# Performance work log

Hardware: AMD Instinct MI355X
Metric: run time of the kernel (lower is better)

The kernel has to match this reference:

```python
import jax, jax.numpy as jnp
import numpy as np

N = 50000        # nodes
E = 500000       # undirected edges (stored once)
D = 64           # n_in_features
DOUT = 64        # n_out_features
HLF = 2          # hl_factor
NCONV = 3        # n_conv_its
H = D * HLF      # hidden width of conv MLPs


def setup_inputs() -> dict:
    key = jax.random.key(0)
    ks = jax.random.split(key, 8)
    s = 0.05
    edge_features = jax.random.normal(ks[0], (E, D), jnp.float32)
    edge_index = jax.random.randint(ks[1], (2, E), 0, N, dtype=jnp.int64)
    node_w1 = jax.random.normal(ks[2], (NCONV, 2 * D, H), jnp.float32) * s
    node_b1 = jnp.zeros((NCONV, H), jnp.float32)
    node_w2 = jax.random.normal(ks[3], (NCONV, H, D), jnp.float32) * s
    node_b2 = jnp.zeros((NCONV, D), jnp.float32)
    edge_w1 = jax.random.normal(ks[4], (2 * D, H), jnp.float32) * s
    edge_b1 = jnp.zeros((H,), jnp.float32)
    edge_w2 = jax.random.normal(ks[5], (H, DOUT), jnp.float32) * s
    edge_b2 = jnp.zeros((DOUT,), jnp.float32)
    return dict(edge_features=edge_features, edge_index=edge_index,
                node_w1=node_w1, node_b1=node_b1, node_w2=node_w2, node_b2=node_b2,
                edge_w1=edge_w1, edge_b1=edge_b1, edge_w2=edge_w2, edge_b2=edge_b2)


def _seg_mean(x, idx, n):
    s = jax.ops.segment_sum(x, idx, num_segments=n)
    c = jax.ops.segment_sum(jnp.ones((idx.shape[0], 1), x.dtype), idx, num_segments=n)
    return s / jnp.maximum(c, 1.0)


def reference(edge_features, edge_index, node_w1, node_b1, node_w2, node_b2,
              edge_w1, edge_b1, edge_w2, edge_b2):
    src, dst = edge_index[0], edge_index[1]
    # bidirectional (symmetrized) edges for message passing
    bi_src = jnp.concatenate([src, dst])
    bi_dst = jnp.concatenate([dst, src])

    # EdgeConvNoNodes: node feature = mean of incident edge features
    x = _seg_mean(jnp.concatenate([edge_features, edge_features], axis=0), bi_dst, N)  # [N, D]

    # NodeConv layers with residual: message = MLP(cat[x_i, x_j]), mean-aggregated
    for i in range(NCONV):
        m = jnp.concatenate([x[bi_dst], x[bi_src]], axis=-1)        # [2E, 2D]
        m = jax.nn.relu(m @ node_w1[i] + node_b1[i])                # [2E, H]
        m = jax.nn.relu(m @ node_w2[i] + node_b2[i])                # [2E, D]
        x = x + _seg_mean(m, bi_dst, N)

    # EdgeConv: symmetric edge MLP over node endpoint pairs + symmetry side loss
    def emlp(a, b):
        h = jax.nn.relu(jnp.concatenate([a, b], axis=-1) @ edge_w1 + edge_b1)
        return h @ edge_w2 + edge_b2

    e1 = emlp(x[src], x[dst])   # [E, DOUT]
    e2 = emlp(x[dst], x[src])   # [E, DOUT]
    edge_out = 0.5 * (e1 + e2)
    side_loss = jnp.mean((e1 - e2) ** 2)
    return edge_out, side_loss
```

## Files before the change

kernel.cpp:

```cpp
#include <hip/hip_runtime.h>


#define NN 50000
#define NE 500000
#define DE 1000000
#define NEB 7813

typedef __attribute__((ext_vector_type(8))) __bf16 bfrag;
typedef __attribute__((ext_vector_type(8))) short  svec8;
typedef __attribute__((ext_vector_type(4))) float  f32x4;

__device__ __forceinline__ unsigned short f2bf(float f){
  unsigned u = __builtin_bit_cast(unsigned, f);
  u += 0x7fffu + ((u >> 16) & 1u);
  return (unsigned short)(u >> 16);
}
__device__ __forceinline__ float bf2f(unsigned short s){
  return __builtin_bit_cast(float, ((unsigned)s) << 16);
}
#define MFMA __builtin_amdgcn_mfma_f32_16x16x32_bf16

__device__ __forceinline__ bfrag hbuild(const unsigned short* __restrict__ p,
                                        const unsigned short* __restrict__ q){
  svec8 pv = *(const svec8*)p;
  svec8 qv = *(const svec8*)q;
  bfrag r;
  #pragma unroll
  for (int i = 0; i < 8; i++){
    float f = bf2f((unsigned short)pv[i]) + bf2f((unsigned short)qv[i]);
    f = f > 0.f ? f : 0.f;
    r[i] = (__bf16)f;
  }
  return r;
}

__global__ void k_hist(const int* __restrict__ ei, int* __restrict__ cnt){
  int e = blockIdx.x*256 + threadIdx.x;
  if (e >= DE) return;
  int dst = (e < NE) ? ei[NE + e] : ei[e - NE];
  atomicAdd(&cnt[dst], 1);
}

__global__ void k_scan(const int* __restrict__ cnt, int* __restrict__ off,
                       int* __restrict__ cur, float* __restrict__ dinv){
  __shared__ int wsum[16];
  __shared__ int carry_s;
  int tid = threadIdx.x;
  int lane = tid & 63, w = tid >> 6;
  int carry = 0;
  for (int base = 0; base < NN; base += 1024){
    int idx = base + tid;
    int v = (idx < NN) ? cnt[idx] : 0;
    int inc = v;
    for (int o2 = 1; o2 < 64; o2 <<= 1){
      int t = __shfl_up(inc, o2);
      if (lane >= o2) inc += t;
    }
    if (lane == 63) wsum[w] = inc;
    __syncthreads();
    if (tid < 16){
      int vv = wsum[tid], p = vv;
      for (int o2 = 1; o2 < 16; o2 <<= 1){
        int t = __shfl_up(p, o2, 16);
        if (tid >= o2) p += t;
      }
      wsum[tid] = p - vv;
    }
    __syncthreads();
    int ex = carry + wsum[w] + inc - v;
    if (idx < NN){
      off[idx] = ex; cur[idx] = ex;
      dinv[idx] = 1.0f / (float)(v > 1 ? v : 1);
    }
    if (tid == 1023) carry_s = carry + wsum[15] + inc;
    __syncthreads();
    carry = carry_s;
  }
  if (tid == 0) off[NN] = DE;
}

__global__ void k_fill(const int* __restrict__ ei, int* __restrict__ cur,
                       int* __restrict__ nbr, int* __restrict__ dstA, int* __restrict__ eid){
  int e = blockIdx.x*256 + threadIdx.x;
  if (e >= DE) return;
  int s, d, id;
  if (e < NE){ s = ei[e];  d = ei[NE + e]; id = e;      }
  else       { s = ei[e];  d = ei[e - NE]; id = e - NE; }
  int pos = atomicAdd(&cur[d], 1);
  nbr[pos] = s; dstA[pos] = d; eid[pos] = id;
}

__global__ void k_pack(const float* __restrict__ nw1, const float* __restrict__ nw2,
                       const float* __restrict__ ew1, const float* __restrict__ ew2,
                       unsigned short* __restrict__ wp){
  int t = blockIdx.x*256 + threadIdx.x;
  if (t >= 98304) return;
  const float* src; int NO, p, base;
  if (t < 49152)      { int l = t/16384;            src = nw1 + l*16384; NO=128; p = t - l*16384;      base = t - p; }
  else if (t < 73728) { int q = t-49152; int l=q/8192; src = nw2 + l*8192; NO=64; p = q - l*8192;      base = t - p; }
  else if (t < 90112) {                              src = ew1;           NO=128; p = t - 73728;       base = 73728; }
  else                {                              src = ew2;           NO=64;  p = t - 90112;       base = 90112; }
  int f = p >> 9, r = p & 511, lane = r >> 3, i = r & 7;
  int NB = NO >> 4, kb = f / NB, nb = f - kb*NB;
  int k = kb*32 + ((lane >> 4) << 3) + i;
  int c = nb*16 + (lane & 15);
  wp[base + p] = f2bf(src[k*NO + c]);
}

__global__ __launch_bounds__(256,4) void k_init(
    const float* __restrict__ ef, const int* __restrict__ dstA,
    const int* __restrict__ eid, float* __restrict__ xsum)
{
  int lane = threadIdx.x & 63, wid = threadIdx.x >> 6;
  int tile = (blockIdx.x*4 + wid) * 32;
  if (tile >= DE) return;
  int q = lane >> 4, c4 = lane & 15;
  int dr = dstA[tile + (lane & 31)];
  int er = eid[tile + (lane & 31)];
  f32x4 v[8];
  #pragma unroll
  for (int it = 0; it < 8; it++){
    int row = q + it*4;
    int e = __shfl(er, row);
    v[it] = *(const f32x4*)(ef + (size_t)e*64 + c4*4);
  }
  int prev = __shfl_up(dr, 1);
  bool flag = (lane < 32) && (lane == 0 || dr != prev);
  unsigned long long mask = __ballot(flag);
  while (mask){
    int s = (int)__builtin_ctzll(mask);
    mask &= mask - 1;
    int e = mask ? (int)__builtin_ctzll(mask) : 32;
    int dseg = __shfl(dr, s);
    f32x4 p = {0,0,0,0};
    #pragma unroll
    for (int it = 0; it < 8; it++){
      int row = q + it*4;
      if ((unsigned)(row - s) < (unsigned)(e - s)) p += v[it];
    }
    #pragma unroll
    for (int k = 0; k < 4; k++){
      p[k] += __shfl_xor(p[k], 16);
      p[k] += __shfl_xor(p[k], 32);
    }
    if (q == 0){
      atomicAdd(&xsum[dseg*64 + c4*4 + 0], p[0]);
      atomicAdd(&xsum[dseg*64 + c4*4 + 1], p[1]);
      atomicAdd(&xsum[dseg*64 + c4*4 + 2], p[2]);
      atomicAdd(&xsum[dseg*64 + c4*4 + 3], p[3]);
    }
  }
}

__global__ void k_div(const float* __restrict__ xsum, const float* __restrict__ dinv,
                      float* __restrict__ x, unsigned short* __restrict__ xbf){
  int n = blockIdx.x*4 + (threadIdx.x >> 6);
  int lane = threadIdx.x & 63;
  if (n >= NN) return;
  float v = xsum[n*64 + lane] * dinv[n];
  x[n*64 + lane] = v;
  xbf[n*64 + lane] = f2bf(v);
}

__global__ __launch_bounds__(256,2) void k_pq(
    const unsigned short* __restrict__ xbf,
    const unsigned short* __restrict__ wp, int w1off,
    const float* __restrict__ bias,
    unsigned short* __restrict__ pb, unsigned short* __restrict__ qb)
{
  int lane = threadIdx.x & 63, wid = threadIdx.x >> 6;
  int tile = (blockIdx.x*4 + wid) * 32;
  if (tile >= NN) return;
  int r16 = lane & 15, g = lane >> 4;
  const svec8* w1g = (const svec8*)(wp + w1off);
  bfrag a[2][2];
  #pragma unroll
  for (int rb = 0; rb < 2; rb++){
    int n = tile + rb*16 + r16; if (n >= NN) n = NN-1;
    #pragma unroll
    for (int kb = 0; kb < 2; kb++)
      a[rb][kb] = __builtin_bit_cast(bfrag, *(const svec8*)(xbf + n*64 + kb*32 + g*8));
  }
  for (int ph = 0; ph < 2; ph++){
    f32x4 acc[8][2];
    #pragma unroll
    for (int nb = 0; nb < 8; nb++){ acc[nb][0] = (f32x4){0,0,0,0}; acc[nb][1] = (f32x4){0,0,0,0}; }
    #pragma unroll
    for (int kb = 0; kb < 2; kb++){
      #pragma unroll
      for (int nb = 0; nb < 8; nb++){
        bfrag b = __builtin_bit_cast(bfrag, w1g[((ph*2+kb)*8+nb)*64 + lane]);
        acc[nb][0] = MFMA(a[0][kb], b, acc[nb][0], 0, 0, 0);
        acc[nb][1] = MFMA(a[1][kb], b, acc[nb][1], 0, 0, 0);
      }
    }
    unsigned short* ob = ph ? qb : pb;
    #pragma unroll
    for (int nb = 0; nb < 8; nb++){
      float bv = (ph == 0) ? bias[nb*16 + r16] : 0.f;
      #pragma unroll
      for (int rb = 0; rb < 2; rb++){
        #pragma unroll
        for (int j = 0; j < 4; j++){
          int n = tile + rb*16 + g*4 + j;
          if (n < NN) ob[n*128 + nb*16 + r16] = f2bf(acc[nb][rb][j] + bv);
        }
      }
    }
  }
}

__global__ __launch_bounds__(256,4) void k_conv(
    const unsigned short* __restrict__ pb, const unsigned short* __restrict__ qb,
    const int* __restrict__ cdst, const int* __restrict__ cnbr,
    const unsigned short* __restrict__ wp, int w2off,
    const float* __restrict__ b2, float* __restrict__ xsum)
{
  int lane = threadIdx.x & 63, wid = threadIdx.x >> 6;
  int tile = (blockIdx.x*4 + wid) * 32;
  if (tile >= DE) return;
  int r16 = lane & 15, g = lane >> 4;
  int dr = cdst[tile + (lane & 31)];
  int d0 = cdst[tile + r16],      d1 = cdst[tile + 16 + r16];
  int s0 = cnbr[tile + r16],      s1 = cnbr[tile + 16 + r16];
  const svec8* w2g = (const svec8*)(wp + w2off);

  f32x4 acc[4][2];
  #pragma unroll
  for (int nb = 0; nb < 4; nb++){ acc[nb][0] = (f32x4){0,0,0,0}; acc[nb][1] = (f32x4){0,0,0,0}; }

  #pragma unroll
  for (int kb = 0; kb < 4; kb++){
    int off = kb*32 + g*8;
    bfrag h0 = hbuild(pb + d0*128 + off, qb + s0*128 + off);
    bfrag h1 = hbuild(pb + d1*128 + off, qb + s1*128 + off);
    #pragma unroll
    for (int nb = 0; nb < 4; nb++){
      bfrag b = __builtin_bit_cast(bfrag, w2g[(kb*4+nb)*64 + lane]);
      acc[nb][0] = MFMA(h0, b, acc[nb][0], 0, 0, 0);
      acc[nb][1] = MFMA(h1, b, acc[nb][1], 0, 0, 0);
    }
  }
  float m[4][2][4];
  #pragma unroll
  for (int nb = 0; nb < 4; nb++){
    float bv = b2[nb*16 + r16];
    #pragma unroll
    for (int rb = 0; rb < 2; rb++){
      #pragma unroll
      for (int j = 0; j < 4; j++){
        float v = acc[nb][rb][j] + bv;
        m[nb][rb][j] = v > 0.f ? v : 0.f;
      }
    }
  }
  int prev = __shfl_up(dr, 1);
  bool flag = (lane < 32) && (lane == 0 || dr != prev);
  unsigned long long mask = __ballot(flag);
  while (mask){
    int s = (int)__builtin_ctzll(mask);
    mask &= mask - 1;
    int e = mask ? (int)__builtin_ctzll(mask) : 32;
    int dseg = __shfl(dr, s);
    float p0 = 0.f, p1 = 0.f, p2 = 0.f, p3 = 0.f;
    #pragma unroll
    for (int rb = 0; rb < 2; rb++){
      #pragma unroll
      for (int j = 0; j < 4; j++){
        int row = rb*16 + g*4 + j;
        if ((unsigned)(row - s) < (unsigned)(e - s)){
          p0 += m[0][rb][j]; p1 += m[1][rb][j]; p2 += m[2][rb][j]; p3 += m[3][rb][j];
        }
      }
    }
    p0 += __shfl_xor(p0, 16); p0 += __shfl_xor(p0, 32);
    p1 += __shfl_xor(p1, 16); p1 += __shfl_xor(p1, 32);
    p2 += __shfl_xor(p2, 16); p2 += __shfl_xor(p2, 32);
    p3 += __shfl_xor(p3, 16); p3 += __shfl_xor(p3, 32);
    if (g == 0){
      atomicAdd(&xsum[dseg*64 +      r16], p0);
      atomicAdd(&xsum[dseg*64 + 16 + r16], p1);
      atomicAdd(&xsum[dseg*64 + 32 + r16], p2);
      atomicAdd(&xsum[dseg*64 + 48 + r16], p3);
    }
  }
}

__global__ void k_finish(const float* __restrict__ xsum, const float* __restrict__ dinv,
                         float* __restrict__ x, unsigned short* __restrict__ xbf){
  int n = blockIdx.x*4 + (threadIdx.x >> 6);
  int lane = threadIdx.x & 63;
  if (n >= NN) return;
  float v = x[n*64 + lane] + xsum[n*64 + lane] * dinv[n];
  x[n*64 + lane] = v;
  xbf[n*64 + lane] = f2bf(v);
}

__global__ __launch_bounds__(256,4) void k_edge(
    const unsigned short* __restrict__ pe, const unsigned short* __restrict__ qe,
    const int* __restrict__ ei,
    const unsigned short* __restrict__ wp,
    const float* __restrict__ b2,
    float* __restrict__ outp, float* __restrict__ part)
{
  __shared__ float wred[4];
  int lane = threadIdx.x & 63, wid = threadIdx.x >> 6;
  int tile = (blockIdx.x*4 + wid) * 16;
  bool valid = tile < NE;
  int tl = valid ? tile : 0;
  int r16 = lane & 15, g = lane >> 4;
  const svec8* w2g = (const svec8*)(wp + 90112);
  int el = tl + r16;
  int sn = ei[el], dn = ei[NE + el];

  f32x4 acc[4][2];
  #pragma unroll
  for (int nb = 0; nb < 4; nb++){ acc[nb][0] = (f32x4){0,0,0,0}; acc[nb][1] = (f32x4){0,0,0,0}; }

  #pragma unroll
  for (int kb = 0; kb < 4; kb++){
    int off = kb*32 + g*8;
    bfrag h0 = hbuild(pe + sn*128 + off, qe + dn*128 + off);
    bfrag h1 = hbuild(pe + dn*128 + off, qe + sn*128 + off);
    #pragma unroll
    for (int nb = 0; nb < 4; nb++){
      bfrag b = __builtin_bit_cast(bfrag, w2g[(kb*4+nb)*64 + lane]);
      acc[nb][0] = MFMA(h0, b, acc[nb][0], 0, 0, 0);
      acc[nb][1] = MFMA(h1, b, acc[nb][1], 0, 0, 0);
    }
  }
  float lsum = 0.f;
  #pragma unroll
  for (int nb = 0; nb < 4; nb++){
    float bv = b2[nb*16 + r16];
    #pragma unroll
    for (int j = 0; j < 4; j++){
      float v1 = acc[nb][0][j] + bv;
      float v2 = acc[nb][1][j] + bv;
      int e = tile + g*4 + j;
      if (valid) outp[e*64 + nb*16 + r16] = 0.5f*(v1 + v2);
      float d = v1 - v2; lsum += d*d;
    }
  }
  if (!valid) lsum = 0.f;
  for (int o2 = 32; o2 > 0; o2 >>= 1) lsum += __shfl_down(lsum, o2);
  if (lane == 0) wred[wid] = lsum;
  __syncthreads();
  if (threadIdx.x == 0) part[blockIdx.x] = wred[0] + wred[1] + wred[2] + wred[3];
}

__global__ void k_final(const float* __restrict__ part, float* __restrict__ outp){
  __shared__ float wred[16];
  int tid = threadIdx.x;
  float s = 0.f;
  for (int i = tid; i < NEB; i += 1024) s += part[i];
  for (int o2 = 32; o2 > 0; o2 >>= 1) s += __shfl_down(s, o2);
  int lane = tid & 63, w = tid >> 6;
  if (lane == 0) wred[w] = s;
  __syncthreads();
  if (tid == 0){
    float t = 0.f;
    #pragma unroll
    for (int i = 0; i < 16; i++) t += wred[i];
    outp[32000000] = t * (1.0f / 32000000.0f);
  }
}

extern "C" void kernel_launch(void* const* d_in, const int* in_sizes, int n_in,
                              void* d_out, int out_size, void* d_ws, size_t ws_size,
                              hipStream_t stream)
{
  const float* ef  = (const float*)d_in[0];
  const int*   ei  = (const int*)  d_in[1];
  const float* nw1 = (const float*)d_in[2];
  const float* nb1 = (const float*)d_in[3];
  const float* nw2 = (const float*)d_in[4];
  const float* nb2 = (const float*)d_in[5];
  const float* ew1 = (const float*)d_in[6];
  const float* eb1 = (const float*)d_in[7];
  const float* ew2 = (const float*)d_in[8];
  const float* eb2 = (const float*)d_in[9];
  float* outp = (float*)d_out;

  char* ws = (char*)d_ws;
  size_t o = 0;
  auto alloc = [&](size_t b)->char*{ char* p = ws + o; o += (b + 255) & ~(size_t)255; return p; };
  int*   cnt  = (int*)  alloc((size_t)NN*4);
  int*   off  = (int*)  alloc((size_t)(NN+1)*4);
  int*   cur  = (int*)  alloc((size_t)NN*4);
  float* dinv = (float*)alloc((size_t)NN*4);
  int*   nbr  = (int*)  alloc((size_t)DE*4);
  int*   dstA = (int*)  alloc((size_t)DE*4);
  int*   eid  = (int*)  alloc((size_t)DE*4);
  float* x    = (float*)alloc((size_t)NN*64*4);
  unsigned short* xbf = (unsigned short*)alloc((size_t)NN*64*2);
  unsigned short* wp  = (unsigned short*)alloc((size_t)98304*2);
  float* part = (float*)alloc((size_t)NEB*4);
  unsigned short* pbuf = (unsigned short*)alloc((size_t)NN*128*2);
  unsigned short* qbuf = (unsigned short*)alloc((size_t)NN*128*2);
  float* xsI  = (float*)alloc((size_t)NN*64*4);
  float* xs0  = (float*)alloc((size_t)NN*64*4);
  float* xs1  = (float*)alloc((size_t)NN*64*4);
  float* xs2  = (float*)alloc((size_t)NN*64*4);
  float* xsum[3] = {xs0, xs1, xs2};

  hipMemsetAsync(cnt, 0, (size_t)NN*4, stream);
  hipMemsetAsync(xsI, 0, (size_t)NN*64*4, stream);
  hipMemsetAsync(xs0, 0, (size_t)NN*64*4, stream);
  hipMemsetAsync(xs1, 0, (size_t)NN*64*4, stream);
  hipMemsetAsync(xs2, 0, (size_t)NN*64*4, stream);
  k_hist<<<(DE+255)/256, 256, 0, stream>>>(ei, cnt);
  k_scan<<<1, 1024, 0, stream>>>(cnt, off, cur, dinv);
  k_fill<<<(DE+255)/256, 256, 0, stream>>>(ei, cur, nbr, dstA, eid);
  k_pack<<<384, 256, 0, stream>>>(nw1, nw2, ew1, ew2, wp);
  k_init<<<NEB, 256, 0, stream>>>(ef, dstA, eid, xsI);
  k_div<<<NN/4 + 1, 256, 0, stream>>>(xsI, dinv, x, xbf);
  for (int l = 0; l < 3; l++){
    k_pq<<<391, 256, 0, stream>>>(xbf, wp, l*16384, nb1 + l*128, pbuf, qbuf);
    k_conv<<<DE/128 + 1, 256, 0, stream>>>(pbuf, qbuf, dstA, nbr, wp,
                                           49152 + l*8192, nb2 + l*64, xsum[l]);
    k_finish<<<NN/4 + 1, 256, 0, stream>>>(xsum[l], dinv, x, xbf);
  }
  k_pq<<<391, 256, 0, stream>>>(xbf, wp, 73728, eb1, pbuf, qbuf);
  k_edge<<<NEB, 256, 0, stream>>>(pbuf, qbuf, ei, wp, eb2, outp, part);
  k_final<<<1, 1024, 0, stream>>>(part, outp);
}
```

Baseline: 700.1 us.

## Interleave P/Q node buffers, sort final edges by source, batch gathers before MFMA

Merges the separate P and Q node projection buffers into one interleaved [N,256] array so each node's P and Q halves sit on adjacent cache lines. Adds a second CSR-style sort of the original edges by source node so the final edge kernel gathers with more locality, then scatters outputs back through a permutation. Hoists all gathers in k_conv and k_edge ahead of the MFMA loop to expose memory-level parallelism, lowering the occupancy hint from 4 to 3 to make room for the extra registers. This adds a histogram, scan and fill pass plus extra index arrays, and the output writes in k_edge become scattered.

Result: slower. 723.4 us (+3.3%).

```diff
diff --git a/kernel.cpp b/kernel.cpp
--- a/kernel.cpp
+++ b/kernel.cpp
@@ -20,10 +20,7 @@
 }
 #define MFMA __builtin_amdgcn_mfma_f32_16x16x32_bf16
 
-__device__ __forceinline__ bfrag hbuild(const unsigned short* __restrict__ p,
-                                        const unsigned short* __restrict__ q){
-  svec8 pv = *(const svec8*)p;
-  svec8 qv = *(const svec8*)q;
+__device__ __forceinline__ bfrag hbuild2(svec8 pv, svec8 qv){
   bfrag r;
   #pragma unroll
   for (int i = 0; i < 8; i++){
@@ -34,15 +31,18 @@
   return r;
 }
 
-__global__ void k_hist(const int* __restrict__ ei, int* __restrict__ cnt){
+__global__ void k_hist(const int* __restrict__ ei, int* __restrict__ cnt,
+                       int* __restrict__ cnt2){
   int e = blockIdx.x*256 + threadIdx.x;
   if (e >= DE) return;
   int dst = (e < NE) ? ei[NE + e] : ei[e - NE];
   atomicAdd(&cnt[dst], 1);
-}
-
-__global__ void k_scan(const int* __restrict__ cnt, int* __restrict__ off,
-                       int* __restrict__ cur, float* __restrict__ dinv){
+  if (e < NE) atomicAdd(&cnt2[ei[e]], 1);
+}
+
+__device__ __forceinline__ void scan_impl(const int* __restrict__ cnt,
+                                          int* __restrict__ off, int* __restrict__ cur,
+                                          float* __restrict__ dinv, int total){
   __shared__ int wsum[16];
   __shared__ int carry_s;
   int tid = threadIdx.x;
@@ -76,11 +76,21 @@
     __syncthreads();
     carry = carry_s;
   }
-  if (tid == 0) off[NN] = DE;
+  if (tid == 0) off[NN] = total;
+}
+
+__global__ void k_scan2(const int* __restrict__ cntA, int* __restrict__ offA,
+                        int* __restrict__ curA, float* __restrict__ dinvA,
+                        const int* __restrict__ cntB, int* __restrict__ offB,
+                        int* __restrict__ curB, float* __restrict__ dinvB){
+  if (blockIdx.x == 0) scan_impl(cntA, offA, curA, dinvA, DE);
+  else                 scan_impl(cntB, offB, curB, dinvB, NE);
 }
 
 __global__ void k_fill(const int* __restrict__ ei, int* __restrict__ cur,
-                       int* __restrict__ nbr, int* __restrict__ dstA, int* __restrict__ eid){
+                       int* __restrict__ nbr, int* __restrict__ dstA, int* __restrict__ eid,
+                       int* __restrict__ cur2, int* __restrict__ eord,
+                       int* __restrict__ es, int* __restrict__ ed){
   int e = blockIdx.x*256 + threadIdx.x;
   if (e >= DE) return;
   int s, d, id;
@@ -88,6 +98,10 @@
   else       { s = ei[e];  d = ei[e - NE]; id = e - NE; }
   int pos = atomicAdd(&cur[d], 1);
   nbr[pos] = s; dstA[pos] = d; eid[pos] = id;
+  if (e < NE){
+    int p2 = atomicAdd(&cur2[s], 1);
+    eord[p2] = e; es[p2] = s; ed[p2] = d;
+  }
 }
 
 __global__ void k_pack(const float* __restrict__ nw1, const float* __restrict__ nw2,
@@ -166,7 +180,7 @@
     const unsigned short* __restrict__ xbf,
     const unsigned short* __restrict__ wp, int w1off,
     const float* __restrict__ bias,
-    unsigned short* __restrict__ pb, unsigned short* __restrict__ qb)
+    unsigned short* __restrict__ pq)
 {
   int lane = threadIdx.x & 63, wid = threadIdx.x >> 6;
   int tile = (blockIdx.x*4 + wid) * 32;
@@ -194,7 +208,7 @@
         acc[nb][1] = MFMA(a[1][kb], b, acc[nb][1], 0, 0, 0);
       }
     }
-    unsigned short* ob = ph ? qb : pb;
+    int half = ph ? 128 : 0;
     #pragma unroll
     for (int nb = 0; nb < 8; nb++){
       float bv = (ph == 0) ? bias[nb*16 + r16] : 0.f;
@@ -203,15 +217,15 @@
         #pragma unroll
         for (int j = 0; j < 4; j++){
           int n = tile + rb*16 + g*4 + j;
-          if (n < NN) ob[n*128 + nb*16 + r16] = f2bf(acc[nb][rb][j] + bv);
+          if (n < NN) pq[(size_t)n*256 + half + nb*16 + r16] = f2bf(acc[nb][rb][j] + bv);
         }
       }
     }
   }
 }
 
-__global__ __launch_bounds__(256,4) void k_conv(
-    const unsigned short* __restrict__ pb, const unsigned short* __restrict__ qb,
+__global__ __launch_bounds__(256,3) void k_conv(
+    const unsigned short* __restrict__ pq,
     const int* __restrict__ cdst, const int* __restrict__ cnbr,
     const unsigned short* __restrict__ wp, int w2off,
     const float* __restrict__ b2, float* __restrict__ xsum)
@@ -225,15 +239,24 @@
   int s0 = cnbr[tile + r16],      s1 = cnbr[tile + 16 + r16];
   const svec8* w2g = (const svec8*)(wp + w2off);
 
-  f32x4 acc[4][2];
-  #pragma unroll
-  for (int nb = 0; nb < 4; nb++){ acc[nb][0] = (f32x4){0,0,0,0}; acc[nb][1] = (f32x4){0,0,0,0}; }
-
+  svec8 LP0[4], LQ0[4], LP1[4], LQ1[4];
   #pragma unroll
   for (int kb = 0; kb < 4; kb++){
     int off = kb*32 + g*8;
-    bfrag h0 = hbuild(pb + d0*128 + off, qb + s0*128 + off);
-    bfrag h1 = hbuild(pb + d1*128 + off, qb + s1*128 + off);
+    LP0[kb] = *(const svec8*)(pq + (size_t)d0*256 + off);
+    LQ0[kb] = *(const svec8*)(pq + (size_t)s0*256 + 128 + off);
+    LP1[kb] = *(const svec8*)(pq + (size_t)d1*256 + off);
+    LQ1[kb] = *(const svec8*)(pq + (size_t)s1*256 + 128 + off);
+  }
+
+  f32x4 acc[4][2];
+  #pragma unroll
+  for (int nb = 0; nb < 4; nb++){ acc[nb][0] = (f32x4){0,0,0,0}; acc[nb][1] = (f32x4){0,0,0,0}; }
+
+  #pragma unroll
+  for (int kb = 0; kb < 4; kb++){
+    bfrag h0 = hbuild2(LP0[kb], LQ0[kb]);
+    bfrag h1 = hbuild2(LP1[kb], LQ1[kb]);
     #pragma unroll
     for (int nb = 0; nb < 4; nb++){
       bfrag b = __builtin_bit_cast(bfrag, w2g[(kb*4+nb)*64 + lane]);
@@ -296,9 +319,9 @@
   xbf[n*64 + lane] = f2bf(v);
 }
 
-__global__ __launch_bounds__(256,4) void k_edge(
-    const unsigned short* __restrict__ pe, const unsigned short* __restrict__ qe,
-    const int* __restrict__ ei,
+__global__ __launch_bounds__(256,3) void k_edge(
+    const unsigned short* __restrict__ pq,
+    const int* __restrict__ eord, const int* __restrict__ es, const int* __restrict__ ed,
     const unsigned short* __restrict__ wp,
     const float* __restrict__ b2,
     float* __restrict__ outp, float* __restrict__ part)
@@ -310,18 +333,27 @@
   int tl = valid ? tile : 0;
   int r16 = lane & 15, g = lane >> 4;
   const svec8* w2g = (const svec8*)(wp + 90112);
-  int el = tl + r16;
-  int sn = ei[el], dn = ei[NE + el];
-
-  f32x4 acc[4][2];
-  #pragma unroll
-  for (int nb = 0; nb < 4; nb++){ acc[nb][0] = (f32x4){0,0,0,0}; acc[nb][1] = (f32x4){0,0,0,0}; }
-
+  int eidv = eord[tl + r16];
+  int sid  = es[tl + r16], did = ed[tl + r16];
+
+  svec8 SP[4], SQ[4], DP[4], DQ[4];
   #pragma unroll
   for (int kb = 0; kb < 4; kb++){
     int off = kb*32 + g*8;
-    bfrag h0 = hbuild(pe + sn*128 + off, qe + dn*128 + off);
-    bfrag h1 = hbuild(pe + dn*128 + off, qe + sn*128 + off);
+    SP[kb] = *(const svec8*)(pq + (size_t)sid*256 + off);
+    SQ[kb] = *(const svec8*)(pq + (size_t)sid*256 + 128 + off);
+    DP[kb] = *(const svec8*)(pq + (size_t)did*256 + off);
+    DQ[kb] = *(const svec8*)(pq + (size_t)did*256 + 128 + off);
+  }
+
+  f32x4 acc[4][2];
+  #pragma unroll
+  for (int nb = 0; nb < 4; nb++){ acc[nb][0] = (f32x4){0,0,0,0}; acc[nb][1] = (f32x4){0,0,0,0}; }
+
+  #pragma unroll
+  for (int kb = 0; kb < 4; kb++){
+    bfrag h0 = hbuild2(SP[kb], DQ[kb]);
+    bfrag h1 = hbuild2(DP[kb], SQ[kb]);
     #pragma unroll
     for (int nb = 0; nb < 4; nb++){
       bfrag b = __builtin_bit_cast(bfrag, w2g[(kb*4+nb)*64 + lane]);
@@ -337,8 +369,8 @@
     for (int j = 0; j < 4; j++){
       float v1 = acc[nb][0][j] + bv;
       float v2 = acc[nb][1][j] + bv;
-      int e = tile + g*4 + j;
-      if (valid) outp[e*64 + nb*16 + r16] = 0.5f*(v1 + v2);
+      int eo = __shfl(eidv, g*4 + j);
+      if (valid) outp[(size_t)eo*64 + nb*16 + r16] = 0.5f*(v1 + v2);
       float d = v1 - v2; lsum += d*d;
     }
   }
@@ -389,39 +421,46 @@
   int*   off  = (int*)  alloc((size_t)(NN+1)*4);
   int*   cur  = (int*)  alloc((size_t)NN*4);
   float* dinv = (float*)alloc((size_t)NN*4);
+  int*   cnt2 = (int*)  alloc((size_t)NN*4);
+  int*   off2 = (int*)  alloc((size_t)(NN+1)*4);
+  int*   cur2 = (int*)  alloc((size_t)NN*4);
+  float* dinvS= (float*)alloc((size_t)NN*4);
   int*   nbr  = (int*)  alloc((size_t)DE*4);
   int*   dstA = (int*)  alloc((size_t)DE*4);
   int*   eid  = (int*)  alloc((size_t)DE*4);
+  int*   eord = (int*)  alloc((size_t)NE*4);
+  int*   es   = (int*)  alloc((size_t)NE*4);
+  int*   ed   = (int*)  alloc((size_t)NE*4);
   float* x    = (float*)alloc((size_t)NN*64*4);
   unsigned short* xbf = (unsigned short*)alloc((size_t)NN*64*2);
   unsigned short* wp  = (unsigned short*)alloc((size_t)98304*2);
   float* part = (float*)alloc((size_t)NEB*4);
-  unsigned short* pbuf = (unsigned short*)alloc((size_t)NN*128*2);
-  unsigned short* qbuf = (unsigned short*)alloc((size_t)NN*128*2);
+  unsigned short* pq  = (unsigned short*)alloc((size_t)NN*256*2);
   float* xsI  = (float*)alloc((size_t)NN*64*4);
   float* xs0  = (float*)alloc((size_t)NN*64*4);
   float* xs1  = (float*)alloc((size_t)NN*64*4);
   float* xs2  = (float*)alloc((size_t)NN*64*4);
   float* xsum[3] = {xs0, xs1, xs2};
 
-  hipMemsetAsync(cnt, 0, (size_t)NN*4, stream);
+  hipMemsetAsync(cnt,  0, (size_t)NN*4, stream);
+  hipMemsetAsync(cnt2, 0, (size_t)NN*4, stream);
   hipMemsetAsync(xsI, 0, (size_t)NN*64*4, stream);
   hipMemsetAsync(xs0, 0, (size_t)NN*64*4, stream);
   hipMemsetAsync(xs1, 0, (size_t)NN*64*4, stream);
   hipMemsetAsync(xs2, 0, (size_t)NN*64*4, stream);
-  k_hist<<<(DE+255)/256, 256, 0, stream>>>(ei, cnt);
-  k_scan<<<1, 1024, 0, stream>>>(cnt, off, cur, dinv);
-  k_fill<<<(DE+255)/256, 256, 0, stream>>>(ei, cur, nbr, dstA, eid);
+  k_hist<<<(DE+255)/256, 256, 0, stream>>>(ei, cnt, cnt2);
+  k_scan2<<<2, 1024, 0, stream>>>(cnt, off, cur, dinv, cnt2, off2, cur2, dinvS);
+  k_fill<<<(DE+255)/256, 256, 0, stream>>>(ei, cur, nbr, dstA, eid, cur2, eord, es, ed);
   k_pack<<<384, 256, 0, stream>>>(nw1, nw2, ew1, ew2, wp);
   k_init<<<NEB, 256, 0, stream>>>(ef, dstA, eid, xsI);
   k_div<<<NN/4 + 1, 256, 0, stream>>>(xsI, dinv, x, xbf);
   for (int l = 0; l < 3; l++){
-    k_pq<<<391, 256, 0, stream>>>(xbf, wp, l*16384, nb1 + l*128, pbuf, qbuf);
-    k_conv<<<DE/128 + 1, 256, 0, stream>>>(pbuf, qbuf, dstA, nbr, wp,
+    k_pq<<<391, 256, 0, stream>>>(xbf, wp, l*16384, nb1 + l*128, pq);
+    k_conv<<<DE/128 + 1, 256, 0, stream>>>(pq, dstA, nbr, wp,
                                            49152 + l*8192, nb2 + l*64, xsum[l]);
     k_finish<<<NN/4 + 1, 256, 0, stream>>>(xsum[l], dinv, x, xbf);
   }
-  k_pq<<<391, 256, 0, stream>>>(xbf, wp, 73728, eb1, pbuf, qbuf);
-  k_edge<<<NEB, 256, 0, stream>>>(pbuf, qbuf, ei, wp, eb2, outp, part);
+  k_pq<<<391, 256, 0, stream>>>(xbf, wp, 73728, eb1, pq);
+  k_edge<<<NEB, 256, 0, stream>>>(pq, eord, es, ed, wp, eb2, outp, part);
   k_final<<<1, 1024, 0, stream>>>(part, outp);
 }
```
